# Kernel optimization log

Hardware: AMD Instinct MI355X
Metric: run time of the kernel (lower is better)

Reference implementation:

```python
import jax, jax.numpy as jnp
import numpy as np

N = 30000
E = 480000
F = 256
H = 32
HEADS = 4
NUM_LABEL = 6
NEG_SLOPE = 0.2
BN_EPS = 1e-5
NUM_ITER = 3
ROUTE_NODES = 2 * (HEADS + HEADS)  # 16
PC_OUT = 8


def squash(t, axis=-1):
    sq = (t ** 2).sum(axis=axis, keepdims=True)
    return (sq / (1.0 + sq)) * t / jnp.sqrt(sq)


def glorot(key, shape):
    fan_in, fan_out = shape[-2], shape[-1]
    s = jnp.sqrt(6.0 / (fan_in + fan_out))
    return jax.random.uniform(key, shape, jnp.float32, -s, s)


def setup_inputs() -> dict:
    key = jax.random.key(0)
    ks = jax.random.split(key, 10)
    x = jax.random.normal(ks[0], (N, F), jnp.float32)
    rng = np.random.default_rng(0)
    src = rng.integers(0, N, E)
    dst = rng.integers(0, N, E)
    dst = np.where(src == dst, (dst + 1) % N, dst)  # no self loops (torch code removes them)
    edge_index = jnp.asarray(np.stack([src, dst]), jnp.int32)
    y = jax.random.randint(ks[1], (N,), 0, NUM_LABEL, jnp.int32)
    return {
        'x': x,
        'gamma': jnp.ones((F,), jnp.float32),
        'beta': jnp.zeros((F,), jnp.float32),
        'W_lin': glorot(ks[2], (F, HEADS * H)),
        'b_lin': jnp.zeros((HEADS * H,), jnp.float32),
        'W_gat': glorot(ks[3], (F, HEADS * H)),
        'att': glorot(ks[4], (1, HEADS, 2 * H)),
        'b_gat': jnp.zeros((HEADS * H,), jnp.float32),
        'Wp': glorot(ks[5], (2, H, PC_OUT)),
        'bp': jnp.zeros((2, PC_OUT), jnp.float32),
        'route_w': jax.random.normal(ks[6], (NUM_LABEL, ROUTE_NODES, PC_OUT, H), jnp.float32),
        'edge_index': edge_index,
        'y': y,
    }


def _forward(x, gamma, beta, W_lin, b_lin, W_gat, att, b_gat, Wp, bp, route_w, edge_index, y):
    n = x.shape[0]
    # BatchNorm1d (training-mode batch statistics, biased variance)
    mean = x.mean(axis=0)
    var = ((x - mean) ** 2).mean(axis=0)
    xb = (x - mean) / jnp.sqrt(var + BN_EPS) * gamma + beta

    hidden = (xb @ W_lin + b_lin).reshape(n, HEADS, H)

    # ---- GATConv (concat=True, add self-loops) ----
    xt = (xb @ W_gat).reshape(n, HEADS, H)
    loop = jnp.arange(n, dtype=edge_index.dtype)
    src = jnp.concatenate([edge_index[0], loop])
    dst = jnp.concatenate([edge_index[1], loop])
    x_i = xt[dst]  # [Et, HEADS, H] target
    x_j = xt[src]  # [Et, HEADS, H] source
    a_i, a_j = att[:, :, :H], att[:, :, H:]
    alpha = (x_i * a_i).sum(-1) + (x_j * a_j).sum(-1)  # [Et, HEADS]
    alpha = jnp.where(alpha >= 0, alpha, NEG_SLOPE * alpha)
    amax = jax.ops.segment_max(alpha, dst, num_segments=n)
    e = jnp.exp(alpha - amax[dst])
    denom = jax.ops.segment_sum(e, dst, num_segments=n)
    alpha = e / (denom[dst] + 1e-16)
    msg = x_j * alpha[:, :, None]
    aggr = jax.ops.segment_sum(msg, dst, num_segments=n)  # [n, HEADS, H]
    gat_out = aggr.reshape(n, HEADS * H) + b_gat

    xc = jnp.concatenate([gat_out.reshape(n, HEADS, H), hidden], axis=1)  # [n, 2*HEADS, H]
    xc = jax.nn.relu(xc)

    # ---- primary capsules: 2 Linear(H->8), cat on route axis, squash ----
    pc = jnp.einsum('nrh,cho->ncro', xc, Wp) + bp[None, :, None, :]  # [n,2,8,8]
    u = squash(pc.reshape(n, ROUTE_NODES, PC_OUT))  # [n,16,8]

    # ---- digit capsules: dynamic routing (softmax over route nodes, dim=2) ----
    priors = jnp.einsum('nri,crio->cnro', u, route_w)  # [6,n,16,H]
    logits = jnp.zeros(priors.shape[:3], priors.dtype)  # [6,n,16]
    for it in range(NUM_ITER):
        probs = jax.nn.softmax(logits, axis=2)
        v = squash((probs[..., None] * priors).sum(axis=2))  # [6,n,H]
        if it != NUM_ITER - 1:
            logits = logits + (priors * v[:, :, None, :]).sum(-1)

    xo = v.transpose(1, 0, 2)  # [n,6,H]
    features = xo.reshape(n, NUM_LABEL * H)
    output = jnp.sqrt((xo ** 2).sum(-1))  # [n,6] capsule lengths
    logp = jax.nn.log_softmax(output, axis=-1)
    loss = -jnp.take_along_axis(logp, y[:, None].astype(jnp.int32), axis=1).mean()
    return output, loss, features


def reference(x, gamma, beta, W_lin, b_lin, W_gat, att, b_gat, Wp, bp, route_w, edge_index, y):
    return _forward(x, gamma, beta, W_lin, b_lin, W_gat, att, b_gat, Wp, bp, route_w, edge_index, y)
```

## Files before the change

### kernel.cpp

```cpp
#include <hip/hip_runtime.h>
#include <hip/hip_bf16.h>

#define NND 30000
#define NE  480000
#define FD  256
#define HD  32
#define HEADS 4
#define NLAB 6
#define NEG_SLOPE 0.2f
#define BN_EPS 1e-5f

#define WS_FLAG      0
#define WS_BNSUM     4
#define WS_BNSQ      260
#define WS_LOSS      516
#define WS_COUNTS    520
#define WS_ZERO_ELEMS 30524
#define WS_OFFSETS   30524
#define WS_CURSOR    60528
#define WS_GAMMA     90528
#define WS_BETA      90784
#define WS_WLIN      91040
#define WS_BLIN      123808
#define WS_WGAT      123936
#define WS_ATT       156704
#define WS_BGAT      156960
#define WS_WP        157088
#define WS_BP        157600
#define WS_RW        157616
#define WS_SCALE     182192
#define WS_SHIFT     182448
#define WS_WC        182704
#define WS_BC        248240
#define WS_SD        248496
#define WS_SS        368496
#define WS_ONORM     488496
#define WS_CSR       668496
#define WS_XF        1178496
#define WS_U         1178496
#define WS_BLKSUM    5018496
#define WS_BLKOFF    5018624
#define WS_Y         8858496
#define WS_XCG       16538496

#define OUT_LOSS_IDX 180000
#define OUT_FEAT_IDX 180001

#define SCAN_NB 118

__device__ __forceinline__ float lrelu(float a) { return a >= 0.0f ? a : NEG_SLOPE * a; }

__device__ __forceinline__ void pin(float& x) { asm volatile("" : "+v"(x)); }

template<int CTRL>
__device__ __forceinline__ float fdpp(float v) {
    return __int_as_float(__builtin_amdgcn_mov_dpp(__float_as_int(v), CTRL, 0xF, 0xF, true));
}
template<int PAT>
__device__ __forceinline__ float fswz(float v) {
    return __int_as_float(__builtin_amdgcn_ds_swizzle(__float_as_int(v), PAT));
}
__device__ __forceinline__ float redq(float v) {
    v += fdpp<0xB1>(v);
    v += fdpp<0x4E>(v);
    v += fswz<0x101F>(v);
    v += fswz<0x201F>(v);
    v += fswz<0x401F>(v);
    return v;
}
__device__ __forceinline__ float redq_sum64(float v) {
    v = redq(v);
    return v + __shfl_xor(v, 32);
}
__device__ __forceinline__ float redq_max64(float v) {
    v = fmaxf(v, fdpp<0xB1>(v));
    v = fmaxf(v, fdpp<0x4E>(v));
    v = fmaxf(v, fswz<0x101F>(v));
    v = fmaxf(v, fswz<0x201F>(v));
    v = fmaxf(v, fswz<0x401F>(v));
    return fmaxf(v, __shfl_xor(v, 32));
}
__device__ __forceinline__ void dreduce(float dp[8], int k, float out[8]) {
    #pragma unroll
    for (int j = 0; j < 8; ++j) {
        dp[j] += fdpp<0xB1>(dp[j]);
        dp[j] += fdpp<0x4E>(dp[j]);
    }
    float A = (k == 0) ? dp[0] : (k == 1) ? dp[1] : (k == 2) ? dp[2] : dp[3];
    float B = (k == 0) ? dp[4] : (k == 1) ? dp[5] : (k == 2) ? dp[6] : dp[7];
    A += fswz<0x101F>(A); A += fswz<0x201F>(A); A += fswz<0x401F>(A);
    B += fswz<0x101F>(B); B += fswz<0x201F>(B); B += fswz<0x401F>(B);
    out[0] = fdpp<0x00>(A); out[1] = fdpp<0x55>(A); out[2] = fdpp<0xAA>(A); out[3] = fdpp<0xFF>(A);
    out[4] = fdpp<0x00>(B); out[5] = fdpp<0x55>(B); out[6] = fdpp<0xAA>(B); out[7] = fdpp<0xFF>(B);
}

__global__ void k_detect(const unsigned int* gamma_raw, int* flag) {
    unsigned int w = gamma_raw[0];
    *flag = ((w & 0xFFFFu) == 0x3F80u) ? 1 : 0;
}

__device__ __forceinline__ float cvt_load(const void* p, int i, int f) {
    if (f) return __bfloat162float(((const __hip_bfloat16*)p)[i]);
    return ((const float*)p)[i];
}

__global__ void k_convert(const void* src, float* dst, int n, const int* flagp) {
    int f = *flagp;
    for (int i = blockIdx.x * blockDim.x + threadIdx.x; i < n; i += gridDim.x * blockDim.x)
        dst[i] = cvt_load(src, i, f);
}

__global__ void k_convert_params(const void* p0, const void* p1, const void* p2, const void* p3,
                                 const void* p4, const void* p5, const void* p6, const void* p7,
                                 const void* p8, const void* p9, float* dst, const int* flagp) {
    int f = *flagp;
    int i = blockIdx.x * blockDim.x + threadIdx.x;
    if (i >= 91664) return;
    const void* p; int off;
    if      (i < 256)   { p = p0; off = i; }
    else if (i < 512)   { p = p1; off = i - 256; }
    else if (i < 33280) { p = p2; off = i - 512; }
    else if (i < 33408) { p = p3; off = i - 33280; }
    else if (i < 66176) { p = p4; off = i - 33408; }
    else if (i < 66432) { p = p5; off = i - 66176; }
    else if (i < 66560) { p = p6; off = i - 66432; }
    else if (i < 67072) { p = p7; off = i - 66560; }
    else if (i < 67088) { p = p8; off = i - 67072; }
    else                { p = p9; off = i - 67088; }
    dst[i] = cvt_load(p, off, f);
}

__global__ void k_bn_stats(const float* xf, float* bn_sum, float* bn_sq) {
    int t = threadIdx.x;
    int rows = (NND + gridDim.x - 1) / gridDim.x;
    int r0 = blockIdx.x * rows;
    int r1 = min(NND, r0 + rows);
    float s = 0.0f, ss = 0.0f;
    for (int r = r0; r < r1; ++r) {
        float v = xf[(size_t)r * FD + t];
        s += v; ss += v * v;
    }
    atomicAdd(&bn_sum[t], s);
    atomicAdd(&bn_sq[t], ss);
}

__global__ void k_bn_final(const float* bn_sum, const float* bn_sq, const float* gamma,
                           const float* beta, float* scale, float* shift) {
    int t = threadIdx.x;
    float mean = bn_sum[t] / (float)NND;
    float var  = bn_sq[t] / (float)NND - mean * mean;
    float inv  = 1.0f / sqrtf(var + BN_EPS);
    float sc   = gamma[t] * inv;
    scale[t] = sc;
    shift[t] = beta[t] - mean * sc;
}

__global__ void k_fold(const float* wlin, const float* wgat, const float* blin,
                       const float* scale, const float* shift, float* Wc, float* bc) {
    int j = blockIdx.x;
    int k = threadIdx.x;
    float w = (j < 128) ? wlin[k * 128 + j] : wgat[k * 128 + (j - 128)];
    Wc[k * 256 + j] = scale[k] * w;
    __shared__ float red[256];
    red[k] = shift[k] * w;
    __syncthreads();
    for (int s = 128; s > 0; s >>= 1) { if (k < s) red[k] += red[k + s]; __syncthreads(); }
    if (k == 0) bc[j] = red[0] + (j < 128 ? blin[j] : 0.0f);
}

__global__ __launch_bounds__(256) void k_gemm(const float* A, const float* B,
                                              const float* bias, float* C) {
    __shared__ __align__(16) float As[16][128];
    __shared__ __align__(16) float Bs[16][64];
    int t  = threadIdx.x;
    int bm = blockIdx.x * 128;
    int bn = blockIdx.y * 64;
    int tr = t / 16, tc = t % 16;
    float acc[8][4] = {};
    int alm = t >> 2;
    int alk = (t & 3) * 4;
    int blk = t >> 4;
    int bln = (t & 15) * 4;
    for (int k0 = 0; k0 < 256; k0 += 16) {
        #pragma unroll
        for (int half = 0; half < 2; ++half) {
            int row = bm + alm + half * 64;
            float4 av = make_float4(0.f, 0.f, 0.f, 0.f);
            if (row < NND) av = *(const float4*)(A + (size_t)row * 256 + k0 + alk);
            int m = alm + half * 64;
            As[alk + 0][m] = av.x; As[alk + 1][m] = av.y;
            As[alk + 2][m] = av.z; As[alk + 3][m] = av.w;
        }
        float4 bv = *(const float4*)(B + (size_t)(k0 + blk) * 256 + bn + bln);
        *(float4*)&Bs[blk][bln] = bv;
        __syncthreads();
        #pragma unroll
        for (int kk = 0; kk < 16; ++kk) {
            float a[8], b[4];
            *(float4*)&a[0] = *(const float4*)&As[kk][tr * 8];
            *(float4*)&a[4] = *(const float4*)&As[kk][tr * 8 + 4];
            *(float4*)&b[0] = *(const float4*)&Bs[kk][tc * 4];
            #pragma unroll
            for (int i = 0; i < 8; ++i)
                #pragma unroll
                for (int j = 0; j < 4; ++j) acc[i][j] += a[i] * b[j];
        }
        __syncthreads();
    }
    #pragma unroll
    for (int i = 0; i < 8; ++i) {
        int row = bm + tr * 8 + i;
        if (row < NND) {
            int col = bn + tc * 4;
            float4 o;
            o.x = acc[i][0] + bias[col + 0];
            o.y = acc[i][1] + bias[col + 1];
            o.z = acc[i][2] + bias[col + 2];
            o.w = acc[i][3] + bias[col + 3];
            *(float4*)(C + (size_t)row * 256 + col) = o;
        }
    }
}

__global__ void k_scores(const float* Y, const float* attf, float* sD, float* sS) {
    int idx = blockIdx.x * blockDim.x + threadIdx.x;
    if (idx >= NND * HEADS) return;
    int n = idx >> 2, h = idx & 3;
    const float* xrow = Y + (size_t)n * 256 + 128 + h * 32;
    const float* ai = attf + h * 64;
    const float* aj = ai + 32;
    float si = 0.f, sj = 0.f;
    #pragma unroll
    for (int k = 0; k < 32; ++k) { float v = xrow[k]; si += v * ai[k]; sj += v * aj[k]; }
    sD[idx] = si; sS[idx] = sj;
}

__global__ void k_count(const int* ei, int* counts) {
    int e = blockIdx.x * blockDim.x + threadIdx.x;
    if (e >= NE + NND) return;
    int d = (e < NE) ? ei[NE + e] : (e - NE);
    atomicAdd(&counts[d], 1);
}

__global__ void k_scan_blk(const int* counts, int* offsets, int* blksum) {
    int t = threadIdx.x, b = blockIdx.x;
    int i = b * 256 + t;
    int v = (i < NND) ? counts[i] : 0;
    int lane = t & 63, wv = t >> 6;
    int x = v;
    #pragma unroll
    for (int off = 1; off < 64; off <<= 1) {
        int y = __shfl_up(x, off);
        if (lane >= off) x += y;
    }
    __shared__ int wsum[4];
    if (lane == 63) wsum[wv] = x;
    __syncthreads();
    int add = 0;
    #pragma unroll
    for (int w = 0; w < 4; ++w) add += (w < wv) ? wsum[w] : 0;
    if (i < NND) offsets[i] = add + x - v;
    if (t == 255) blksum[b] = add + x;
}

__global__ void k_scan_top(const int* blksum, int* blkoff) {
    int t = threadIdx.x;
    int v = (t < SCAN_NB) ? blksum[t] : 0;
    int lane = t & 63, wv = t >> 6;
    int x = v;
    #pragma unroll
    for (int off = 1; off < 64; off <<= 1) {
        int y = __shfl_up(x, off);
        if (lane >= off) x += y;
    }
    __shared__ int ws2[2];
    if (lane == 63) ws2[wv] = x;
    __syncthreads();
    int add = (wv == 1) ? ws2[0] : 0;
    if (t < SCAN_NB) blkoff[t] = add + x - v;
}

__global__ void k_scan_add(const int* blkoff, int* offsets, int* cursor) {
    int i = blockIdx.x * 256 + threadIdx.x;
    if (i >= NND) return;
    int o = offsets[i] + blkoff[blockIdx.x];
    offsets[i] = o;
    cursor[i] = o;
}

__global__ void k_scatter(const int* ei, int* cursor, int* csr) {
    int e = blockIdx.x * blockDim.x + threadIdx.x;
    if (e >= NE + NND) return;
    int s, d;
    if (e < NE) { s = ei[e]; d = ei[NE + e]; } else { s = d = e - NE; }
    int pos = atomicAdd(&cursor[d], 1);
    csr[pos] = s;
}

__global__ __launch_bounds__(256) void k_aggr(const float* Y, const float* sD, const float* sS,
                                              const int* offsets, const int* counts, const int* csr,
                                              const float* bgat, float* xcg) {
    int wave = (blockIdx.x * blockDim.x + threadIdx.x) >> 6;
    int lane = threadIdx.x & 63;
    if (wave >= NND) return;
    int n = wave;
    int start = offsets[n], deg = counts[n];
    float4 sd = *(const float4*)(sD + (size_t)n * 4);
    float m0 = -1e30f, m1 = -1e30f, m2 = -1e30f, m3 = -1e30f;
    for (int e = lane; e < deg; e += 64) {
        int s = csr[start + e];
        float4 sj = *(const float4*)(sS + (size_t)s * 4);
        m0 = fmaxf(m0, lrelu(sd.x + sj.x));
        m1 = fmaxf(m1, lrelu(sd.y + sj.y));
        m2 = fmaxf(m2, lrelu(sd.z + sj.z));
        m3 = fmaxf(m3, lrelu(sd.w + sj.w));
    }
    m0 = redq_max64(m0); m1 = redq_max64(m1);
    m2 = redq_max64(m2); m3 = redq_max64(m3);
    float s0 = 0.f, s1 = 0.f, s2 = 0.f, s3 = 0.f;
    for (int e = lane; e < deg; e += 64) {
        int s = csr[start + e];
        float4 sj = *(const float4*)(sS + (size_t)s * 4);
        s0 += __expf(lrelu(sd.x + sj.x) - m0);
        s1 += __expf(lrelu(sd.y + sj.y) - m1);
        s2 += __expf(lrelu(sd.z + sj.z) - m2);
        s3 += __expf(lrelu(sd.w + sj.w) - m3);
    }
    s0 = redq_sum64(s0); s1 = redq_sum64(s1);
    s2 = redq_sum64(s2); s3 = redq_sum64(s3);
    float i0 = 1.0f / (s0 + 1e-16f), i1 = 1.0f / (s1 + 1e-16f);
    float i2 = 1.0f / (s2 + 1e-16f), i3 = 1.0f / (s3 + 1e-16f);
    float acc0 = 0.f, acc1 = 0.f;
    int hA = lane >> 5;
    for (int base = 0; base < deg; base += 64) {
        int cnt = min(64, deg - base);
        int sidx = 0; float w0 = 0.f, w1 = 0.f, w2 = 0.f, w3 = 0.f;
        if (base + lane < deg) {
            sidx = csr[start + base + lane];
            float4 sj = *(const float4*)(sS + (size_t)sidx * 4);
            w0 = __expf(lrelu(sd.x + sj.x) - m0) * i0;
            w1 = __expf(lrelu(sd.y + sj.y) - m1) * i1;
            w2 = __expf(lrelu(sd.z + sj.z) - m2) * i2;
            w3 = __expf(lrelu(sd.w + sj.w) - m3) * i3;
        }
        for (int j = 0; j < cnt; ++j) {
            int s2i = __builtin_amdgcn_readlane(sidx, j);
            float wa0 = __int_as_float(__builtin_amdgcn_readlane(__float_as_int(w0), j));
            float wa1 = __int_as_float(__builtin_amdgcn_readlane(__float_as_int(w1), j));
            float wb0 = __int_as_float(__builtin_amdgcn_readlane(__float_as_int(w2), j));
            float wb1 = __int_as_float(__builtin_amdgcn_readlane(__float_as_int(w3), j));
            float wA = hA ? wa1 : wa0;
            float wB = hA ? wb1 : wb0;
            const float* xrow = Y + (size_t)s2i * 256 + 128;
            acc0 += wA * xrow[lane];
            acc1 += wB * xrow[64 + lane];
        }
    }
    float r0 = acc0 + bgat[lane];
    float r1 = acc1 + bgat[64 + lane];
    xcg[(size_t)n * 128 + lane]      = r0 > 0.f ? r0 : 0.f;
    xcg[(size_t)n * 128 + 64 + lane] = r1 > 0.f ? r1 : 0.f;
}

__global__ __launch_bounds__(256, 4) void k_u(const float* Y, const float* xcg,
                                              const float* Wpf, const float* bpf, float* uG) {
    int lane = threadIdx.x & 63;
    int gw = blockIdx.x * 4 + (threadIdx.x >> 6);
    int nwaves = gridDim.x * 4;
    int r = lane >> 3, oo = lane & 7;
    float wpA[32], wpB[32];
    #pragma unroll
    for (int k = 0; k < 32; ++k) {
        wpA[k] = Wpf[k * 8 + oo];
        wpB[k] = Wpf[256 + k * 8 + oo];
    }
    #pragma unroll
    for (int k = 0; k < 32; ++k) { pin(wpA[k]); pin(wpB[k]); }
    float bpA = bpf[oo], bpB = bpf[8 + oo];
    for (int n = gw; n < NND; n += nwaves) {
        const float* rowp = (r < 4) ? (xcg + (size_t)n * 128 + r * 32)
                                    : (Y + (size_t)n * 256 + (r - 4) * 32);
        float pcA = bpA, pcB = bpB;
        #pragma unroll
        for (int k4 = 0; k4 < 8; ++k4) {
            float4 xv = *(const float4*)(rowp + k4 * 4);
            xv.x = fmaxf(xv.x, 0.f); xv.y = fmaxf(xv.y, 0.f);
            xv.z = fmaxf(xv.z, 0.f); xv.w = fmaxf(xv.w, 0.f);
            pcA += xv.x * wpA[k4*4+0] + xv.y * wpA[k4*4+1] + xv.z * wpA[k4*4+2] + xv.w * wpA[k4*4+3];
            pcB += xv.x * wpB[k4*4+0] + xv.y * wpB[k4*4+1] + xv.z * wpB[k4*4+2] + xv.w * wpB[k4*4+3];
        }
        float sA = pcA * pcA, sB = pcB * pcB;
        sA += fdpp<0xB1>(sA); sA += fdpp<0x4E>(sA); sA += fswz<0x101F>(sA);
        sB += fdpp<0xB1>(sB); sB += fdpp<0x4E>(sB); sB += fswz<0x101F>(sB);
        float cA = sqrtf(sA) / (1.0f + sA);
        float cB = sqrtf(sB) / (1.0f + sB);
        uG[(size_t)n * 128 + lane]      = pcA * cA;
        uG[(size_t)n * 128 + 64 + lane] = pcB * cB;
    }
}

__global__ __launch_bounds__(256, 3) void k_route3(const float* uG, const float* rwf,
                                                   float* onorm, void* dout, const int* flagp) {
    int flag = *flagp;
    int t = threadIdx.x;
    int lane = t & 63;
    int c = blockIdx.x % 6;
    int wv = t >> 6;
    int widx = (blockIdx.x / 6) * 4 + wv;
    int nstep = (gridDim.x / 6) * 4;
    int h = lane >> 5, o = lane & 31;
    int k = lane & 3;
    float rw[8][8];
    #pragma unroll
    for (int j = 0; j < 8; ++j)
        #pragma unroll
        for (int i = 0; i < 8; ++i)
            rw[j][i] = rwf[(((c * 16) + (h * 8 + j)) * 8 + i) * 32 + o];
    #pragma unroll
    for (int j = 0; j < 8; ++j)
        #pragma unroll
        for (int i = 0; i < 8; ++i)
            pin(rw[j][i]);
    float* outf = (float*)dout;
    __hip_bfloat16* outb = (__hip_bfloat16*)dout;
    for (int n = widx; n < NND; n += nstep) {
        const float* up = uG + (size_t)n * 128 + h * 64;
        float p[8];
        #pragma unroll
        for (int j = 0; j < 8; ++j) {
            float4 a = *(const float4*)(up + j * 8);
            float4 b = *(const float4*)(up + j * 8 + 4);
            p[j] = a.x*rw[j][0] + a.y*rw[j][1] + a.z*rw[j][2] + a.w*rw[j][3]
                 + b.x*rw[j][4] + b.y*rw[j][5] + b.z*rw[j][6] + b.w*rw[j][7];
        }
        float tl = p[0]+p[1]+p[2]+p[3]+p[4]+p[5]+p[6]+p[7];
        float s = (tl + __shfl_xor(tl, 32)) * 0.0625f;
        float sq = redq(s * s);
        float v = s * (sqrtf(sq) / (1.0f + sq));
        float logits[8], dp[8];
        #pragma unroll
        for (int j = 0; j < 8; ++j) dp[j] = p[j] * v;
        dreduce(dp, k, logits);
        float sq3 = 0.f, v3 = 0.f;
        #pragma unroll
        for (int it = 0; it < 2; ++it) {
            float mx = logits[0];
            #pragma unroll
            for (int j = 1; j < 8; ++j) mx = fmaxf(mx, logits[j]);
            mx = fmaxf(mx, __shfl_xor(mx, 32));
            float e[8]; float se = 0.f;
            #pragma unroll
            for (int j = 0; j < 8; ++j) { e[j] = __expf(logits[j] - mx); se += e[j]; }
            se += __shfl_xor(se, 32);
            float inv = 1.0f / se;
            float sl = 0.f;
            #pragma unroll
            for (int j = 0; j < 8; ++j) sl += e[j] * p[j];
            sl *= inv;
            float ss = sl + __shfl_xor(sl, 32);
            float q = redq(ss * ss);
            float vv = ss * (sqrtf(q) / (1.0f + q));
            if (it == 0) {
                float dd[8], lu[8];
                #pragma unroll
                for (int j = 0; j < 8; ++j) dd[j] = p[j] * vv;
                dreduce(dd, k, lu);
                #pragma unroll
                for (int j = 0; j < 8; ++j) logits[j] += lu[j];
            } else { v3 = vv; sq3 = q; }
        }
        if (lane < 32) {
            size_t fidx = (size_t)OUT_FEAT_IDX + (size_t)n * 192 + c * 32 + o;
            if (flag) outb[fidx] = __float2bfloat16(v3); else outf[fidx] = v3;
            if (lane == 0) {
                float norm = sq3 / (1.0f + sq3);
                onorm[n * 6 + c] = norm;
                size_t oidx = (size_t)n * 6 + c;
                if (flag) outb[oidx] = __float2bfloat16(norm); else outf[oidx] = norm;
            }
        }
    }
}

__global__ void k_loss(const float* onorm, const int* y, float* acc) {
    float l = 0.f;
    for (int n = blockIdx.x * blockDim.x + threadIdx.x; n < NND; n += gridDim.x * blockDim.x) {
        const float* v = onorm + n * 6;
        float m = v[0];
        #pragma unroll
        for (int cc = 1; cc < 6; ++cc) m = fmaxf(m, v[cc]);
        float s = 0.f;
        #pragma unroll
        for (int cc = 0; cc < 6; ++cc) s += expf(v[cc] - m);
        l += m + logf(s) - v[y[n]];
    }
    __shared__ float red[256];
    red[threadIdx.x] = l;
    __syncthreads();
    for (int s = 128; s > 0; s >>= 1) { if (threadIdx.x < s) red[threadIdx.x] += red[threadIdx.x + s]; __syncthreads(); }
    if (threadIdx.x == 0) atomicAdd(acc, red[0]);
}

__global__ void k_loss_fin(const float* acc, void* dout, const int* flagp) {
    float v = acc[0] / (float)NND;
    if (*flagp) ((__hip_bfloat16*)dout)[OUT_LOSS_IDX] = __float2bfloat16(v);
    else        ((float*)dout)[OUT_LOSS_IDX] = v;
}

extern "C" void kernel_launch(void* const* d_in, const int* in_sizes, int n_in,
                              void* d_out, int out_size, void* d_ws, size_t ws_size,
                              hipStream_t stream) {
    (void)in_sizes; (void)n_in; (void)out_size; (void)ws_size;
    float* ws = (float*)d_ws;
    int*  wsi = (int*)d_ws;
    const int* ei = (const int*)d_in[11];
    const int* y  = (const int*)d_in[12];

    hipMemsetAsync(d_ws, 0, (size_t)WS_ZERO_ELEMS * 4, stream);
    k_detect<<<1, 1, 0, stream>>>((const unsigned int*)d_in[1], wsi + WS_FLAG);

    k_convert<<<2048, 256, 0, stream>>>(d_in[0], ws + WS_XF, NND * FD, wsi + WS_FLAG);
    k_convert_params<<<(91664 + 255) / 256, 256, 0, stream>>>(
        d_in[1], d_in[2], d_in[3], d_in[4], d_in[5], d_in[6], d_in[7], d_in[8], d_in[9], d_in[10],
        ws + WS_GAMMA, wsi + WS_FLAG);

    k_bn_stats<<<120, 256, 0, stream>>>(ws + WS_XF, ws + WS_BNSUM, ws + WS_BNSQ);
    k_bn_final<<<1, 256, 0, stream>>>(ws + WS_BNSUM, ws + WS_BNSQ, ws + WS_GAMMA, ws + WS_BETA,
                                      ws + WS_SCALE, ws + WS_SHIFT);
    k_fold<<<256, 256, 0, stream>>>(ws + WS_WLIN, ws + WS_WGAT, ws + WS_BLIN,
                                    ws + WS_SCALE, ws + WS_SHIFT, ws + WS_WC, ws + WS_BC);

    k_gemm<<<dim3((NND + 127) / 128, 4), 256, 0, stream>>>(ws + WS_XF, ws + WS_WC, ws + WS_BC, ws + WS_Y);

    k_scores<<<(NND * HEADS + 255) / 256, 256, 0, stream>>>(ws + WS_Y, ws + WS_ATT, ws + WS_SD, ws + WS_SS);

    k_count<<<(NE + NND + 255) / 256, 256, 0, stream>>>(ei, wsi + WS_COUNTS);
    k_scan_blk<<<SCAN_NB, 256, 0, stream>>>(wsi + WS_COUNTS, wsi + WS_OFFSETS, wsi + WS_BLKSUM);
    k_scan_top<<<1, 128, 0, stream>>>(wsi + WS_BLKSUM, wsi + WS_BLKOFF);
    k_scan_add<<<SCAN_NB, 256, 0, stream>>>(wsi + WS_BLKOFF, wsi + WS_OFFSETS, wsi + WS_CURSOR);
    k_scatter<<<(NE + NND + 255) / 256, 256, 0, stream>>>(ei, wsi + WS_CURSOR, wsi + WS_CSR);

    k_aggr<<<(NND + 3) / 4, 256, 0, stream>>>(ws + WS_Y, ws + WS_SD, ws + WS_SS,
                                              wsi + WS_OFFSETS, wsi + WS_COUNTS, wsi + WS_CSR,
                                              ws + WS_BGAT, ws + WS_XCG);

    k_u<<<512, 256, 0, stream>>>(ws + WS_Y, ws + WS_XCG, ws + WS_WP, ws + WS_BP, ws + WS_U);
    k_route3<<<3072, 256, 0, stream>>>(ws + WS_U, ws + WS_RW, ws + WS_ONORM, d_out, wsi + WS_FLAG);

    k_loss<<<118, 256, 0, stream>>>(ws + WS_ONORM, y, ws + WS_LOSS);
    k_loss_fin<<<1, 1, 0, stream>>>(ws + WS_LOSS, d_out, wsi + WS_FLAG);
}
```

Baseline: 543.5 us.

## Stream transposed route and primary-capsule weights from cache instead of registers

Adds a prep kernel that transposes route_w and Wp into contiguous per-lane layouts in workspace. The k_u and routing kernels now read those weights as float4 loads inside the node loop instead of pinning 64 weights per thread in registers. Dropping the register pinning and the occupancy hints is meant to raise occupancy, and the routing grid becomes contiguous per class with twice as many blocks. The cost is extra global and L1/L2 weight traffic on every node iteration plus one additional launch.

```diff
diff --git a/kernel.cpp b/kernel.cpp
--- a/kernel.cpp
+++ b/kernel.cpp
@@ -40,6 +40,8 @@
 #define WS_U         1178496
 #define WS_BLKSUM    5018496
 #define WS_BLKOFF    5018624
+#define WS_RWT       248496
+#define WS_WPT       273072
 #define WS_Y         8858496
 #define WS_XCG       16538496
 
@@ -49,8 +51,6 @@
 #define SCAN_NB 118
 
 __device__ __forceinline__ float lrelu(float a) { return a >= 0.0f ? a : NEG_SLOPE * a; }
-
-__device__ __forceinline__ void pin(float& x) { asm volatile("" : "+v"(x)); }
 
 template<int CTRL>
 __device__ __forceinline__ float fdpp(float v) {
@@ -130,6 +130,18 @@
     dst[i] = cvt_load(p, off, f);
 }
 
+__global__ void k_prep(const float* rwf, const float* Wpf, float* rwT, float* wpT) {
+    int idx = blockIdx.x * blockDim.x + threadIdx.x;
+    if (idx < 24576) {
+        int i = idx & 7, r = (idx >> 3) & 15, o = (idx >> 7) & 31, c = idx >> 12;
+        rwT[idx] = rwf[(((c * 16) + r) * 8 + i) * 32 + o];
+    } else if (idx < 24576 + 512) {
+        int f2 = idx - 24576;
+        int k = f2 & 31, oo = (f2 >> 5) & 7, cc = f2 >> 8;
+        wpT[f2] = Wpf[cc * 256 + k * 8 + oo];
+    }
+}
+
 __global__ void k_bn_stats(const float* xf, float* bn_sum, float* bn_sq) {
     int t = threadIdx.x;
     int rows = (NND + gridDim.x - 1) / gridDim.x;
@@ -362,20 +374,14 @@
     xcg[(size_t)n * 128 + 64 + lane] = r1 > 0.f ? r1 : 0.f;
 }
 
-__global__ __launch_bounds__(256, 4) void k_u(const float* Y, const float* xcg,
-                                              const float* Wpf, const float* bpf, float* uG) {
+__global__ __launch_bounds__(256) void k_u(const float* Y, const float* xcg,
+                                           const float* wpT, const float* bpf, float* uG) {
     int lane = threadIdx.x & 63;
     int gw = blockIdx.x * 4 + (threadIdx.x >> 6);
     int nwaves = gridDim.x * 4;
     int r = lane >> 3, oo = lane & 7;
-    float wpA[32], wpB[32];
-    #pragma unroll
-    for (int k = 0; k < 32; ++k) {
-        wpA[k] = Wpf[k * 8 + oo];
-        wpB[k] = Wpf[256 + k * 8 + oo];
-    }
-    #pragma unroll
-    for (int k = 0; k < 32; ++k) { pin(wpA[k]); pin(wpB[k]); }
+    const float* wA = wpT + oo * 32;
+    const float* wB = wpT + 256 + oo * 32;
     float bpA = bpf[oo], bpB = bpf[8 + oo];
     for (int n = gw; n < NND; n += nwaves) {
         const float* rowp = (r < 4) ? (xcg + (size_t)n * 128 + r * 32)
@@ -384,10 +390,12 @@
         #pragma unroll
         for (int k4 = 0; k4 < 8; ++k4) {
             float4 xv = *(const float4*)(rowp + k4 * 4);
+            float4 wa = *(const float4*)(wA + k4 * 4);
+            float4 wb = *(const float4*)(wB + k4 * 4);
             xv.x = fmaxf(xv.x, 0.f); xv.y = fmaxf(xv.y, 0.f);
             xv.z = fmaxf(xv.z, 0.f); xv.w = fmaxf(xv.w, 0.f);
-            pcA += xv.x * wpA[k4*4+0] + xv.y * wpA[k4*4+1] + xv.z * wpA[k4*4+2] + xv.w * wpA[k4*4+3];
-            pcB += xv.x * wpB[k4*4+0] + xv.y * wpB[k4*4+1] + xv.z * wpB[k4*4+2] + xv.w * wpB[k4*4+3];
+            pcA += xv.x * wa.x + xv.y * wa.y + xv.z * wa.z + xv.w * wa.w;
+            pcB += xv.x * wb.x + xv.y * wb.y + xv.z * wb.z + xv.w * wb.w;
         }
         float sA = pcA * pcA, sB = pcB * pcB;
         sA += fdpp<0xB1>(sA); sA += fdpp<0x4E>(sA); sA += fswz<0x101F>(sA);
@@ -399,28 +407,19 @@
     }
 }
 
-__global__ __launch_bounds__(256, 3) void k_route3(const float* uG, const float* rwf,
-                                                   float* onorm, void* dout, const int* flagp) {
+__global__ __launch_bounds__(256) void k_route4(const float* uG, const float* rwT,
+                                                float* onorm, void* dout, const int* flagp) {
     int flag = *flagp;
     int t = threadIdx.x;
     int lane = t & 63;
-    int c = blockIdx.x % 6;
+    int c = blockIdx.x >> 10;
+    int chunk = blockIdx.x & 1023;
     int wv = t >> 6;
-    int widx = (blockIdx.x / 6) * 4 + wv;
-    int nstep = (gridDim.x / 6) * 4;
+    int widx = chunk * 4 + wv;
+    const int nstep = 4096;
     int h = lane >> 5, o = lane & 31;
     int k = lane & 3;
-    float rw[8][8];
-    #pragma unroll
-    for (int j = 0; j < 8; ++j)
-        #pragma unroll
-        for (int i = 0; i < 8; ++i)
-            rw[j][i] = rwf[(((c * 16) + (h * 8 + j)) * 8 + i) * 32 + o];
-    #pragma unroll
-    for (int j = 0; j < 8; ++j)
-        #pragma unroll
-        for (int i = 0; i < 8; ++i)
-            pin(rw[j][i]);
+    const float* rwp = rwT + ((size_t)(c * 32 + o) * 16 + h * 8) * 8;
     float* outf = (float*)dout;
     __hip_bfloat16* outb = (__hip_bfloat16*)dout;
     for (int n = widx; n < NND; n += nstep) {
@@ -428,10 +427,12 @@
         float p[8];
         #pragma unroll
         for (int j = 0; j < 8; ++j) {
-            float4 a = *(const float4*)(up + j * 8);
-            float4 b = *(const float4*)(up + j * 8 + 4);
-            p[j] = a.x*rw[j][0] + a.y*rw[j][1] + a.z*rw[j][2] + a.w*rw[j][3]
-                 + b.x*rw[j][4] + b.y*rw[j][5] + b.z*rw[j][6] + b.w*rw[j][7];
+            float4 a  = *(const float4*)(up + j * 8);
+            float4 b  = *(const float4*)(up + j * 8 + 4);
+            float4 ra = *(const float4*)(rwp + j * 8);
+            float4 rb = *(const float4*)(rwp + j * 8 + 4);
+            p[j] = a.x*ra.x + a.y*ra.y + a.z*ra.z + a.w*ra.w
+                 + b.x*rb.x + b.y*rb.y + b.z*rb.z + b.w*rb.w;
         }
         float tl = p[0]+p[1]+p[2]+p[3]+p[4]+p[5]+p[6]+p[7];
         float s = (tl + __shfl_xor(tl, 32)) * 0.0625f;
@@ -544,8 +545,11 @@
                                               wsi + WS_OFFSETS, wsi + WS_COUNTS, wsi + WS_CSR,
                                               ws + WS_BGAT, ws + WS_XCG);
 
-    k_u<<<512, 256, 0, stream>>>(ws + WS_Y, ws + WS_XCG, ws + WS_WP, ws + WS_BP, ws + WS_U);
-    k_route3<<<3072, 256, 0, stream>>>(ws + WS_U, ws + WS_RW, ws + WS_ONORM, d_out, wsi + WS_FLAG);
+    k_prep<<<(24576 + 512 + 255) / 256, 256, 0, stream>>>(ws + WS_RW, ws + WS_WP,
+                                                          ws + WS_RWT, ws + WS_WPT);
+
+    k_u<<<512, 256, 0, stream>>>(ws + WS_Y, ws + WS_XCG, ws + WS_WPT, ws + WS_BP, ws + WS_U);
+    k_route4<<<6144, 256, 0, stream>>>(ws + WS_U, ws + WS_RWT, ws + WS_ONORM, d_out, wsi + WS_FLAG);
 
     k_loss<<<118, 256, 0, stream>>>(ws + WS_ONORM, y, ws + WS_LOSS);
     k_loss_fin<<<1, 1, 0, stream>>>(ws + WS_LOSS, d_out, wsi + WS_FLAG);
```

Measured after the change: 805.3 us. 48.2% more time.
